# Optimization experiments

Hardware: AMD Instinct MI355X
Metric: run time of the kernel (lower is better)

Reference implementation:

```python
import jax, jax.numpy as jnp
import numpy as np

HIDDEN = 2048
HEADS = 16
HEAD_DIM = HIDDEN // HEADS
GS = 0.1          # governance_strength
ROPE_BASE = 10000.0


def _rope_tables(seq_len, dtype=jnp.float32):
    inv_freq = 1.0 / (ROPE_BASE ** (jnp.arange(0, HEAD_DIM, 2, dtype=jnp.float32) / HEAD_DIM))
    t = jnp.arange(seq_len, dtype=jnp.float32)
    freqs = jnp.outer(t, inv_freq)                      # [S, head_dim/2]
    return jnp.cos(freqs).astype(dtype), jnp.sin(freqs).astype(dtype)


def _apply_rope(x, cos, sin):
    # x: [B, S, H, Dh]; cos/sin: [S, Dh/2] -> broadcast over batch and heads
    c = cos[None, :, None, :]
    s = sin[None, :, None, :]
    x1, x2 = jnp.split(x, 2, axis=-1)
    return jnp.concatenate([x1 * c - x2 * s, x2 * c + x1 * s], axis=-1)


def setup_inputs() -> dict:
    key = jax.random.key(0)
    ks = jax.random.split(key, 9)
    B, S = 2, 1024
    x = jax.random.normal(ks[0], (B, S, HIDDEN), dtype=jnp.float32)
    prophetic_mask = jax.random.normal(ks[1], (B, HEADS, S, S), dtype=jnp.float32)
    policy_mask = jax.random.normal(ks[2], (B, HEADS, S, S), dtype=jnp.float32)
    memory_weights = jax.random.uniform(ks[3], (B, HEADS, S, S), dtype=jnp.float32)
    sd = 1.0 / np.sqrt(HIDDEN)
    Wq = jax.random.normal(ks[4], (HIDDEN, HIDDEN), dtype=jnp.float32) * sd
    Wk = jax.random.normal(ks[5], (HIDDEN, HIDDEN), dtype=jnp.float32) * sd
    Wv = jax.random.normal(ks[6], (HIDDEN, HIDDEN), dtype=jnp.float32) * sd
    Wo = jax.random.normal(ks[7], (HIDDEN, HIDDEN), dtype=jnp.float32) * sd
    bo = jax.random.normal(ks[8], (HIDDEN,), dtype=jnp.float32) * 0.01
    return {"x": x, "prophetic_mask": prophetic_mask, "policy_mask": policy_mask,
            "memory_weights": memory_weights, "Wq": Wq, "Wk": Wk, "Wv": Wv,
            "Wo": Wo, "bo": bo}


def reference(x, prophetic_mask, policy_mask, memory_weights, Wq, Wk, Wv, Wo, bo):
    B, S, D = x.shape
    scale = HEAD_DIM ** -0.5
    # QKV projections (bias=False)
    q = (x @ Wq).reshape(B, S, HEADS, HEAD_DIM)
    k = (x @ Wk).reshape(B, S, HEADS, HEAD_DIM)
    v = (x @ Wv).reshape(B, S, HEADS, HEAD_DIM)
    cos, sin = _rope_tables(S, x.dtype)
    q = _apply_rope(q, cos, sin)
    k = _apply_rope(k, cos, sin)
    # [B, H, S, Dh]
    q = q.transpose(0, 2, 1, 3)
    k = k.transpose(0, 2, 1, 3)
    v = v.transpose(0, 2, 1, 3)
    scores = jnp.einsum('bhqd,bhkd->bhqk', q, k) * scale
    # Combined governance bias: prophetic*gs*0.5 + policy*gs + log(1 + mem*gs + 1e-8)
    bias = (prophetic_mask * (GS * 0.5)
            + policy_mask * GS
            + jnp.log(1.0 + memory_weights * GS + 1e-8))
    scores = scores + bias
    causal = jnp.tril(jnp.ones((S, S), dtype=bool))  # [S, S]
    scores = jnp.where(causal[None, None], scores, -jnp.inf)
    attn = jax.nn.softmax(scores, axis=-1)
    out = jnp.einsum('bhqk,bhkd->bhqd', attn, v)
    out = out.transpose(0, 2, 1, 3).reshape(B, S, D)
    return out @ Wo + bo
```

## Files before the change

### kernel.cpp

```cpp
#include <hip/hip_runtime.h>

typedef unsigned int u32;
typedef unsigned short u16;
typedef __bf16 bf16x8 __attribute__((ext_vector_type(8)));
typedef float f32x4 __attribute__((ext_vector_type(4)));

#define HIDDEN 2048
#define HEADS 16
#define HDIM 128
#define SEQ 1024
#define BATCH 2
#define ROWS (BATCH*SEQ)
#define SCALE 0.08838834764831845f
#define GSC 0.1f

__device__ __forceinline__ u16 f2bf(float f) {
    u32 x = __builtin_bit_cast(u32, f);
    x += 0x7fffu + ((x >> 16) & 1u);
    return (u16)(x >> 16);
}
__device__ __forceinline__ float bf2f(u16 u) {
    return __builtin_bit_cast(float, ((u32)u) << 16);
}
__device__ __forceinline__ void gld_lds16(const void* g, void* l) {
    __builtin_amdgcn_global_load_lds((const __attribute__((address_space(1))) u32*)g,
                                     (__attribute__((address_space(3))) u32*)l, 16, 0, 0);
}

__global__ __launch_bounds__(256) void k_prep(
    const float* __restrict__ x, u16* __restrict__ xb,
    const float* __restrict__ W0, const float* __restrict__ W1,
    const float* __restrict__ W2, const float* __restrict__ W3,
    u16* __restrict__ T0, u16* __restrict__ T1, u16* __restrict__ T2, u16* __restrict__ T3,
    float* __restrict__ cosT, float* __restrict__ sinT) {
    __shared__ float t[32][33];
    const int bid = blockIdx.x;
    const int tid = threadIdx.x;
    if (bid < 4096) {
        const int i = (bid * 256 + tid) * 4;
        float4 v = *(const float4*)(x + i);
        uint2 r;
        r.x = (u32)f2bf(v.x) | ((u32)f2bf(v.y) << 16);
        r.y = (u32)f2bf(v.z) | ((u32)f2bf(v.w) << 16);
        *(uint2*)(xb + i) = r;
    } else if (bid < 4096 + 16384) {
        const int idx = bid - 4096;
        const int bx = (idx & 63) * 32, by = ((idx >> 6) & 63) * 32, z = idx >> 12;
        const float* W = (z == 0) ? W0 : (z == 1) ? W1 : (z == 2) ? W2 : W3;
        u16* Wt = (z == 0) ? T0 : (z == 1) ? T1 : (z == 2) ? T2 : T3;
        const int tx = tid & 31, ty = tid >> 5;
#pragma unroll
        for (int yy = 0; yy < 32; yy += 8)
            t[ty + yy][tx] = W[(size_t)(by + ty + yy) * HIDDEN + bx + tx];
        __syncthreads();
#pragma unroll
        for (int yy = 0; yy < 32; yy += 8)
            Wt[(size_t)(bx + ty + yy) * HIDDEN + by + tx] = f2bf(t[tx][ty + yy]);
    } else {
        const int i = (bid - 20480) * 256 + tid;
        const int s = i >> 6, d = i & 63;
        const float inv = expf(-(float)d * 0.14391156831f);
        const float fr = (float)s * inv;
        cosT[i] = cosf(fr);
        sinT[i] = sinf(fr);
    }
}

__global__ __launch_bounds__(512, 2) void k_qkv(
    const u16* __restrict__ Ag, const u16* __restrict__ Bg,
    u16* __restrict__ qo, u16* __restrict__ ko, u16* __restrict__ vo) {
    __shared__ __align__(16) u16 As[2][16384];
    __shared__ __align__(16) u16 Bs[2][16384];
    const int tid = threadIdx.x;
    const int l = tid & 63, wid = tid >> 6;
    const int wr = wid >> 2, wc = wid & 3;
    const int g = l >> 4, l15 = l & 15;
    const int bid = blockIdx.x;
    const int idx = bid >> 3;
    const int nt = (bid & 7) * 3 + idx % 3;
    const int mt = idx / 3;
    const int m0 = mt * 256, n0 = nt * 256;
    const int swxe = (l15 & 7) << 3;
    int srow[4], scol[4];
#pragma unroll
    for (int p = 0; p < 4; ++p) {
        const int o = p * 8192 + tid * 16;
        const int r = o >> 7;
        srow[p] = r;
        scol[p] = ((o & 127) ^ ((r & 7) << 4)) >> 1;
    }
    f32x4 acc[8][4] = {};
    constexpr int NT = HIDDEN / 64;

#pragma unroll
    for (int p = 0; p < 4; ++p)
        gld_lds16(Ag + (size_t)(m0 + srow[p]) * HIDDEN + scol[p], &As[0][p * 4096 + tid * 8]);
#pragma unroll
    for (int p = 0; p < 4; ++p)
        gld_lds16(Bg + (size_t)(n0 + srow[p]) * HIDDEN + scol[p], &Bs[0][p * 4096 + tid * 8]);
    __syncthreads();

    for (int i = 0; i < NT; ++i) {
        const int cur = i & 1, nb = cur ^ 1;
        if (i + 1 < NT) {
            const int kk1 = (i + 1) * 64;
#pragma unroll
            for (int p = 0; p < 4; ++p)
                gld_lds16(Ag + (size_t)(m0 + srow[p]) * HIDDEN + kk1 + scol[p],
                          &As[nb][p * 4096 + tid * 8]);
#pragma unroll
            for (int p = 0; p < 4; ++p)
                gld_lds16(Bg + (size_t)(n0 + srow[p]) * HIDDEN + kk1 + scol[p],
                          &Bs[nb][p * 4096 + tid * 8]);
        }
        bf16x8 bfr[4][2];
#pragma unroll
        for (int n = 0; n < 4; ++n)
#pragma unroll
            for (int ks = 0; ks < 2; ++ks)
                bfr[n][ks] = *(const bf16x8*)&Bs[cur][(wc * 64 + n * 16 + l15) * 64 +
                                                      ((ks * 32 + g * 8) ^ swxe)];
#pragma unroll
        for (int m = 0; m < 8; ++m) {
            bf16x8 a0 = *(const bf16x8*)&As[cur][(wr * 128 + m * 16 + l15) * 64 +
                                                 ((g * 8) ^ swxe)];
            bf16x8 a1 = *(const bf16x8*)&As[cur][(wr * 128 + m * 16 + l15) * 64 +
                                                 ((32 + g * 8) ^ swxe)];
#pragma unroll
            for (int n = 0; n < 4; ++n) {
                acc[m][n] = __builtin_amdgcn_mfma_f32_16x16x32_bf16(a0, bfr[n][0], acc[m][n], 0, 0, 0);
                acc[m][n] = __builtin_amdgcn_mfma_f32_16x16x32_bf16(a1, bfr[n][1], acc[m][n], 0, 0, 0);
            }
        }
        __syncthreads();
    }
    u16* Cb = (nt < 8) ? qo : (nt < 16) ? ko : vo;
    const int nloc = n0 & 2047;
#pragma unroll
    for (int m = 0; m < 8; ++m)
#pragma unroll
        for (int n = 0; n < 4; ++n) {
            const int col = nloc + wc * 64 + n * 16 + l15;
#pragma unroll
            for (int j = 0; j < 4; ++j) {
                const int row = m0 + wr * 128 + m * 16 + g * 4 + j;
                Cb[(size_t)row * HIDDEN + col] = f2bf(acc[m][n][j]);
            }
        }
}

__global__ __launch_bounds__(256) void k_mid(
    u16* __restrict__ q, u16* __restrict__ k,
    const float* __restrict__ cosT, const float* __restrict__ sinT,
    const u16* __restrict__ v, u16* __restrict__ vT) {
    __shared__ u16 t[32][33];
    const int bid = blockIdx.x;
    const int tid = threadIdx.x;
    if (bid < 8192) {
        const int i = bid * 256 + tid;
        const int row = i >> 10;
        const int hd = i & 1023;
        const int h = hd >> 6, d = hd & 63;
        const int s = row & (SEQ - 1);
        const float c = cosT[s * 64 + d], sn = sinT[s * 64 + d];
        const size_t o1 = (size_t)row * HIDDEN + h * HDIM + d;
        const size_t o2 = o1 + 64;
        float x1 = bf2f(q[o1]), x2 = bf2f(q[o2]);
        q[o1] = f2bf(x1 * c - x2 * sn);
        q[o2] = f2bf(x2 * c + x1 * sn);
        float y1 = bf2f(k[o1]), y2 = bf2f(k[o2]);
        k[o1] = f2bf(y1 * c - y2 * sn);
        k[o2] = f2bf(y2 * c + y1 * sn);
    } else {
        const int idx = bid - 8192;
        const int s0 = (idx & 31) * 32, d0 = ((idx >> 5) & 3) * 32, bh = idx >> 7;
        const int b = bh >> 4, h = bh & 15;
        const int tx = tid & 31, ty = tid >> 5;
#pragma unroll
        for (int yy = 0; yy < 32; yy += 8)
            t[ty + yy][tx] = v[(size_t)(b * SEQ + s0 + ty + yy) * HIDDEN + h * HDIM + d0 + tx];
        __syncthreads();
#pragma unroll
        for (int yy = 0; yy < 32; yy += 8)
            vT[((size_t)bh * HDIM + d0 + ty + yy) * SEQ + s0 + tx] = t[tx][ty + yy];
    }
}

__global__ __launch_bounds__(256) void k_bias(
    const float* __restrict__ pm, const float* __restrict__ po, const float* __restrict__ mw,
    u16* __restrict__ bias) {
    const int j = blockIdx.x;
    const int y = j & 31;
    const int qs = j >> 5;
    const int qt = (qs < 8) ? qs : 23 - qs;
    const int nch = (qt + 1) * 16;
    const int tid = threadIdx.x;
    if (tid >= nch) return;
    const size_t base = ((size_t)y * SEQ + qt * 64) * SEQ + tid * 4;
#pragma unroll 1
    for (int r = 0; r < 64; r += 4) {
        float4 a[4], bq[4], c[4];
#pragma unroll
        for (int rr = 0; rr < 4; ++rr) {
            const size_t off = base + (size_t)(r + rr) * SEQ;
            a[rr]  = *(const float4*)(pm + off);
            bq[rr] = *(const float4*)(po + off);
            c[rr]  = *(const float4*)(mw + off);
        }
#pragma unroll
        for (int rr = 0; rr < 4; ++rr) {
            const size_t off = base + (size_t)(r + rr) * SEQ;
            float v0 = a[rr].x * (GSC * 0.5f) + bq[rr].x * GSC + __logf(fmaf(c[rr].x, GSC, 1.0f + 1e-8f));
            float v1 = a[rr].y * (GSC * 0.5f) + bq[rr].y * GSC + __logf(fmaf(c[rr].y, GSC, 1.0f + 1e-8f));
            float v2 = a[rr].z * (GSC * 0.5f) + bq[rr].z * GSC + __logf(fmaf(c[rr].z, GSC, 1.0f + 1e-8f));
            float v3 = a[rr].w * (GSC * 0.5f) + bq[rr].w * GSC + __logf(fmaf(c[rr].w, GSC, 1.0f + 1e-8f));
            uint2 pk;
            pk.x = (u32)f2bf(v0) | ((u32)f2bf(v1) << 16);
            pk.y = (u32)f2bf(v2) | ((u32)f2bf(v3) << 16);
            *(uint2*)(bias + off) = pk;
        }
    }
}

__global__ __launch_bounds__(128) void k_attn(
    const u16* __restrict__ qraw, const u16* __restrict__ kraw, const u16* __restrict__ vT,
    const u16* __restrict__ bias, u16* __restrict__ attnb) {
    __shared__ __align__(16) u16 Ks[64 * 128];
    __shared__ __align__(16) u16 Vs[128 * 64];
    __shared__ __align__(16) u16 Pl[2][16 * 72];
    const int tid = threadIdx.x;
    const int ln = tid & 63, w = tid >> 6;
    const int g = ln >> 4, q15 = ln & 15;
    const int j = blockIdx.x;
    const int p = j >> 3;
    const int y = (j & 7) * 4 + (p & 3);
    const int t = p >> 2;
    const int hi = t >> 3, lo = t & 7;
    const int qb = hi * 8 + ((hi & 1) ? 7 - lo : lo);
    const int b = y >> 4, h = y & 15;
    const int q0 = qb * 32;
    const int qw = q0 + w * 16;
    const int qg = qw + q15;
    const int ktmax = qb >> 1;
    const int k_r = tid >> 4;
    const int k_c = ((tid & 15) * 8) ^ ((k_r & 7) << 3);
    const int v_r = tid >> 3;
    const int v_c = ((tid & 7) * 8) ^ ((v_r & 7) << 3);
    const int sw = (q15 & 7) << 3;
    bf16x8 qf[4];
    {
        const size_t qoff = (size_t)(b * SEQ + qg) * HIDDEN + h * HDIM;
#pragma unroll
        for (int ds = 0; ds < 4; ++ds) qf[ds] = *(const bf16x8*)(qraw + qoff + ds * 32 + g * 8);
    }
    f32x4 acc_o[8] = {};
    float m_run = -1e30f, l_run = 0.f;
    u16* pw = &Pl[w][0];
    const u16* krow = kraw + (size_t)(b * SEQ) * HIDDEN + h * HDIM;
    const u16* vrow = vT + (size_t)y * HDIM * SEQ;
    const u16* brow = bias + ((size_t)y * SEQ + qg) * SEQ + g * 4;

    uint2 bA[4], bB[4];
    auto issue_bias = [&](uint2 (&bb)[4], int kt) {
        const u16* p0 = brow + kt * 64;
#pragma unroll
        for (int m = 0; m < 4; ++m) bb[m] = *(const uint2*)(p0 + m * 16);
    };

    auto step = [&](int kt, uint2 (&cur)[4], uint2 (&nxt)[4]) {
        const int k0 = kt * 64;
#pragma unroll
        for (int c = 0; c < 8; ++c)
            gld_lds16(krow + (size_t)(k0 + c * 8 + k_r) * HIDDEN + k_c, &Ks[c * 1024 + tid * 8]);
#pragma unroll
        for (int c = 0; c < 8; ++c)
            gld_lds16(vrow + (size_t)(c * 16 + v_r) * SEQ + k0 + v_c, &Vs[c * 1024 + tid * 8]);
        __syncthreads();
        f32x4 accs[4] = {};
#pragma unroll
        for (int ds = 0; ds < 4; ++ds)
#pragma unroll
            for (int m = 0; m < 4; ++m) {
                bf16x8 kf = *(const bf16x8*)&Ks[(m * 16 + q15) * 128 + ((ds * 32 + g * 8) ^ sw)];
                accs[m] = __builtin_amdgcn_mfma_f32_16x16x32_bf16(kf, qf[ds], accs[m], 0, 0, 0);
            }
        if (kt < ktmax) issue_bias(nxt, kt + 1);
        float pmax = -1e30f;
#pragma unroll
        for (int m = 0; m < 4; ++m) {
            const u32 w0 = cur[m].x, w1 = cur[m].y;
            const float bv[4] = { bf2f((u16)(w0 & 0xffff)), bf2f((u16)(w0 >> 16)),
                                  bf2f((u16)(w1 & 0xffff)), bf2f((u16)(w1 >> 16)) };
#pragma unroll
            for (int r = 0; r < 4; ++r) {
                const int kglob = k0 + m * 16 + g * 4 + r;
                float s = (kglob <= qg) ? fmaf(accs[m][r], SCALE, bv[r]) : -1e30f;
                accs[m][r] = s;
                pmax = fmaxf(pmax, s);
            }
        }
        pmax = fmaxf(pmax, __shfl_xor(pmax, 16));
        pmax = fmaxf(pmax, __shfl_xor(pmax, 32));
        const float mnew = fmaxf(m_run, pmax);
        const float alpha = __expf(m_run - mnew);
        float lsum = 0.f;
#pragma unroll
        for (int m = 0; m < 4; ++m)
#pragma unroll
            for (int r = 0; r < 4; ++r) {
                float e = __expf(accs[m][r] - mnew);
                accs[m][r] = e;
                lsum += e;
            }
        lsum += __shfl_xor(lsum, 16);
        lsum += __shfl_xor(lsum, 32);
        l_run = l_run * alpha + lsum;
        m_run = mnew;
#pragma unroll
        for (int m = 0; m < 4; ++m) {
            uint2 pk;
            pk.x = (u32)f2bf(accs[m][0]) | ((u32)f2bf(accs[m][1]) << 16);
            pk.y = (u32)f2bf(accs[m][2]) | ((u32)f2bf(accs[m][3]) << 16);
            *(uint2*)&pw[q15 * 72 + m * 16 + g * 4] = pk;
        }
        float al[4];
#pragma unroll
        for (int jj = 0; jj < 4; ++jj) al[jj] = __shfl(alpha, g * 4 + jj);
#pragma unroll
        for (int n = 0; n < 8; ++n)
#pragma unroll
            for (int jj = 0; jj < 4; ++jj) acc_o[n][jj] *= al[jj];
#pragma unroll
        for (int c = 0; c < 2; ++c) {
            const bf16x8 af = *(const bf16x8*)&pw[q15 * 72 + c * 32 + g * 8];
#pragma unroll
            for (int n = 0; n < 8; ++n) {
                const bf16x8 vf = *(const bf16x8*)&Vs[(n * 16 + q15) * 64 + ((c * 32 + g * 8) ^ sw)];
                acc_o[n] = __builtin_amdgcn_mfma_f32_16x16x32_bf16(af, vf, acc_o[n], 0, 0, 0);
            }
        }
        __syncthreads();
    };

    issue_bias(bA, 0);
    int kt = 0;
    for (;;) {
        step(kt, bA, bB);
        if (kt == ktmax) break;
        ++kt;
        step(kt, bB, bA);
        if (kt == ktmax) break;
        ++kt;
    }

    const float linv = 1.0f / l_run;
    float li[4];
#pragma unroll
    for (int jj = 0; jj < 4; ++jj) li[jj] = __shfl(linv, g * 4 + jj);
#pragma unroll
    for (int n = 0; n < 8; ++n)
#pragma unroll
        for (int jj = 0; jj < 4; ++jj) {
            const int row = b * SEQ + qw + g * 4 + jj;
            const int col = h * HDIM + n * 16 + q15;
            attnb[(size_t)row * HIDDEN + col] = f2bf(acc_o[n][jj] * li[jj]);
        }
}

__global__ __launch_bounds__(256) void k_out(
    const u16* __restrict__ A, const u16* __restrict__ Bt,
    float* __restrict__ Cf, const float* __restrict__ bias) {
    constexpr int K = HIDDEN, N = HIDDEN;
    __shared__ __align__(16) u16 As[128 * 64];
    __shared__ __align__(16) u16 Bs[128 * 64];
    const int tid = threadIdx.x;
    const int ln = tid & 63, w = tid >> 6;
    const int wr = w >> 1, wc = w & 1;
    const int g = ln >> 4, l15 = ln & 15;
    const int m0 = blockIdx.x * 128, n0 = blockIdx.y * 128;
    const int srow = tid >> 3, scol = (tid & 7) * 8;
    f32x4 acc[4][4] = {};
    for (int kk = 0; kk < K; kk += 64) {
#pragma unroll
        for (int c = 0; c < 4; ++c) {
            gld_lds16(A + (size_t)(m0 + c * 32 + srow) * K + kk + scol, &As[c * 2048 + tid * 8]);
            gld_lds16(Bt + (size_t)(n0 + c * 32 + srow) * K + kk + scol, &Bs[c * 2048 + tid * 8]);
        }
        __syncthreads();
#pragma unroll
        for (int ks = 0; ks < 2; ++ks) {
            bf16x8 a[4], b[4];
#pragma unroll
            for (int m = 0; m < 4; ++m)
                a[m] = *(const bf16x8*)&As[(wr * 64 + m * 16 + l15) * 64 + ks * 32 + g * 8];
#pragma unroll
            for (int n = 0; n < 4; ++n)
                b[n] = *(const bf16x8*)&Bs[(wc * 64 + n * 16 + l15) * 64 + ks * 32 + g * 8];
#pragma unroll
            for (int m = 0; m < 4; ++m)
#pragma unroll
                for (int n = 0; n < 4; ++n)
                    acc[m][n] = __builtin_amdgcn_mfma_f32_16x16x32_bf16(a[m], b[n], acc[m][n], 0, 0, 0);
        }
        __syncthreads();
    }
#pragma unroll
    for (int m = 0; m < 4; ++m)
#pragma unroll
        for (int n = 0; n < 4; ++n) {
            const int col = n0 + wc * 64 + n * 16 + l15;
#pragma unroll
            for (int j = 0; j < 4; ++j) {
                const int row = m0 + wr * 64 + m * 16 + g * 4 + j;
                Cf[(size_t)row * N + col] = acc[m][n][j] + bias[col];
            }
        }
}

extern "C" void kernel_launch(void* const* d_in, const int* in_sizes, int n_in,
                              void* d_out, int out_size, void* d_ws, size_t ws_size,
                              hipStream_t stream) {
    (void)in_sizes; (void)n_in; (void)out_size; (void)ws_size;
    const float* x  = (const float*)d_in[0];
    const float* pm = (const float*)d_in[1];
    const float* po = (const float*)d_in[2];
    const float* mw = (const float*)d_in[3];
    const float* Wq = (const float*)d_in[4];
    const float* Wk = (const float*)d_in[5];
    const float* Wv = (const float*)d_in[6];
    const float* Wo = (const float*)d_in[7];
    const float* bo = (const float*)d_in[8];
    float* out = (float*)d_out;

    char* ws = (char*)d_ws;
    const size_t SZ = (size_t)ROWS * HIDDEN;
    const size_t OFF = SZ * 2;
    u16* xb    = (u16*)(ws + 0 * OFF);
    u16* Wqt   = (u16*)(ws + 1 * OFF);
    u16* Wkt   = (u16*)(ws + 2 * OFF);
    u16* Wvt   = (u16*)(ws + 3 * OFF);
    u16* Wot   = (u16*)(ws + 4 * OFF);
    u16* qrawp = (u16*)(ws + 5 * OFF);
    u16* krawp = (u16*)(ws + 6 * OFF);
    u16* vrawp = (u16*)(ws + 7 * OFF);
    u16* vTp   = (u16*)(ws + 8 * OFF);
    u16* attnb = (u16*)(ws + 9 * OFF);
    float* cosT = (float*)(ws + 10 * OFF);
    float* sinT = (float*)(ws + 10 * OFF + 262144);
    u16* biasb  = (u16*)(ws + 11 * OFF);

    k_prep<<<dim3(20736), 256, 0, stream>>>(x, xb, Wq, Wk, Wv, Wo,
                                            Wqt, Wkt, Wvt, Wot, cosT, sinT);
    k_qkv<<<dim3(192), 512, 0, stream>>>(xb, Wqt, qrawp, krawp, vrawp);
    k_mid<<<dim3(12288), 256, 0, stream>>>(qrawp, krawp, cosT, sinT, vrawp, vTp);
    k_bias<<<dim3(512), 256, 0, stream>>>(pm, po, mw, biasb);
    k_attn<<<dim3(1024), 128, 0, stream>>>(qrawp, krawp, vTp, biasb, attnb);
    k_out<<<dim3(16, 16), 256, 0, stream>>>(attnb, Wot, out, bo);
}
```

Measured before the change: 259.0 us.

## Rebalance bias kernel grid and double-buffer swizzled LDS in output GEMM

The bias kernel now gives each block 16 query rows, with rows-per-thread work proportional to the causal width, launched over 2048 blocks instead of 512. This replaces the old 64-row tiles in which many threads sat idle. The output projection GEMM gains double-buffered LDS with prefetch of the next k-tile, an XOR swizzle against LDS bank conflicts, and a remapped 1D grid for better tile locality. The changes target memory-bound bias generation and load/compute serialization in the GEMM, at the cost of twice the LDS use in k_out.

```diff
diff --git a/kernel.cpp b/kernel.cpp
--- a/kernel.cpp
+++ b/kernel.cpp
@@ -190,35 +190,29 @@
     const float* __restrict__ pm, const float* __restrict__ po, const float* __restrict__ mw,
     u16* __restrict__ bias) {
     const int j = blockIdx.x;
+    const int t = 63 - (j >> 5);
     const int y = j & 31;
-    const int qs = j >> 5;
-    const int qt = (qs < 8) ? qs : 23 - qs;
-    const int nch = (qt + 1) * 16;
-    const int tid = threadIdx.x;
-    if (tid >= nch) return;
-    const size_t base = ((size_t)y * SEQ + qt * 64) * SEQ + tid * 4;
-#pragma unroll 1
-    for (int r = 0; r < 64; r += 4) {
-        float4 a[4], bq[4], c[4];
-#pragma unroll
-        for (int rr = 0; rr < 4; ++rr) {
-            const size_t off = base + (size_t)(r + rr) * SEQ;
-            a[rr]  = *(const float4*)(pm + off);
-            bq[rr] = *(const float4*)(po + off);
-            c[rr]  = *(const float4*)(mw + off);
-        }
-#pragma unroll
-        for (int rr = 0; rr < 4; ++rr) {
-            const size_t off = base + (size_t)(r + rr) * SEQ;
-            float v0 = a[rr].x * (GSC * 0.5f) + bq[rr].x * GSC + __logf(fmaf(c[rr].x, GSC, 1.0f + 1e-8f));
-            float v1 = a[rr].y * (GSC * 0.5f) + bq[rr].y * GSC + __logf(fmaf(c[rr].y, GSC, 1.0f + 1e-8f));
-            float v2 = a[rr].z * (GSC * 0.5f) + bq[rr].z * GSC + __logf(fmaf(c[rr].z, GSC, 1.0f + 1e-8f));
-            float v3 = a[rr].w * (GSC * 0.5f) + bq[rr].w * GSC + __logf(fmaf(c[rr].w, GSC, 1.0f + 1e-8f));
-            uint2 pk;
-            pk.x = (u32)f2bf(v0) | ((u32)f2bf(v1) << 16);
-            pk.y = (u32)f2bf(v2) | ((u32)f2bf(v3) << 16);
-            *(uint2*)(bias + off) = pk;
-        }
+    const int row = t * 16 + (threadIdx.x >> 4);
+    const int c0 = threadIdx.x & 15;
+    const int C = 4 * t + 4;
+    const size_t rbase = ((size_t)y * SEQ + row) * SEQ;
+    const float* pr = pm + rbase;
+    const float* qr = po + rbase;
+    const float* mr = mw + rbase;
+    u16* br = bias + rbase;
+#pragma unroll 2
+    for (int c = c0; c < C; c += 16) {
+        const float4 a = *(const float4*)(pr + c * 4);
+        const float4 b = *(const float4*)(qr + c * 4);
+        const float4 m = *(const float4*)(mr + c * 4);
+        float v0 = a.x * (GSC * 0.5f) + b.x * GSC + __logf(fmaf(m.x, GSC, 1.0f + 1e-8f));
+        float v1 = a.y * (GSC * 0.5f) + b.y * GSC + __logf(fmaf(m.y, GSC, 1.0f + 1e-8f));
+        float v2 = a.z * (GSC * 0.5f) + b.z * GSC + __logf(fmaf(m.z, GSC, 1.0f + 1e-8f));
+        float v3 = a.w * (GSC * 0.5f) + b.w * GSC + __logf(fmaf(m.w, GSC, 1.0f + 1e-8f));
+        uint2 pk;
+        pk.x = (u32)f2bf(v0) | ((u32)f2bf(v1) << 16);
+        pk.y = (u32)f2bf(v2) | ((u32)f2bf(v3) << 16);
+        *(uint2*)(br + c * 4) = pk;
     }
 }
 
@@ -370,37 +364,65 @@
 __global__ __launch_bounds__(256) void k_out(
     const u16* __restrict__ A, const u16* __restrict__ Bt,
     float* __restrict__ Cf, const float* __restrict__ bias) {
-    constexpr int K = HIDDEN, N = HIDDEN;
-    __shared__ __align__(16) u16 As[128 * 64];
-    __shared__ __align__(16) u16 Bs[128 * 64];
+    __shared__ __align__(16) u16 As[2][8192];
+    __shared__ __align__(16) u16 Bs[2][8192];
     const int tid = threadIdx.x;
-    const int ln = tid & 63, w = tid >> 6;
-    const int wr = w >> 1, wc = w & 1;
-    const int g = ln >> 4, l15 = ln & 15;
-    const int m0 = blockIdx.x * 128, n0 = blockIdx.y * 128;
-    const int srow = tid >> 3, scol = (tid & 7) * 8;
+    const int l = tid & 63, wid = tid >> 6;
+    const int wr = wid >> 1, wc = wid & 1;
+    const int g = l >> 4, l15 = l & 15;
+    const int bid = blockIdx.x;
+    const int rr = (bid & 7) * 32 + (bid >> 3);
+    const int mt = rr >> 4, nt = rr & 15;
+    const int m0 = mt * 128, n0 = nt * 128;
+    const int swxe = (l15 & 7) << 3;
+    int srow[4], scol[4];
+#pragma unroll
+    for (int p = 0; p < 4; ++p) {
+        const int o = p * 4096 + tid * 16;
+        const int r = o >> 7;
+        srow[p] = r;
+        scol[p] = ((o & 127) ^ ((r & 7) << 4)) >> 1;
+    }
     f32x4 acc[4][4] = {};
-    for (int kk = 0; kk < K; kk += 64) {
-#pragma unroll
-        for (int c = 0; c < 4; ++c) {
-            gld_lds16(A + (size_t)(m0 + c * 32 + srow) * K + kk + scol, &As[c * 2048 + tid * 8]);
-            gld_lds16(Bt + (size_t)(n0 + c * 32 + srow) * K + kk + scol, &Bs[c * 2048 + tid * 8]);
-        }
-        __syncthreads();
-#pragma unroll
-        for (int ks = 0; ks < 2; ++ks) {
-            bf16x8 a[4], b[4];
-#pragma unroll
-            for (int m = 0; m < 4; ++m)
-                a[m] = *(const bf16x8*)&As[(wr * 64 + m * 16 + l15) * 64 + ks * 32 + g * 8];
-#pragma unroll
-            for (int n = 0; n < 4; ++n)
-                b[n] = *(const bf16x8*)&Bs[(wc * 64 + n * 16 + l15) * 64 + ks * 32 + g * 8];
-#pragma unroll
-            for (int m = 0; m < 4; ++m)
-#pragma unroll
-                for (int n = 0; n < 4; ++n)
-                    acc[m][n] = __builtin_amdgcn_mfma_f32_16x16x32_bf16(a[m], b[n], acc[m][n], 0, 0, 0);
+    constexpr int NT = HIDDEN / 64;
+
+#pragma unroll
+    for (int p = 0; p < 4; ++p) {
+        gld_lds16(A + (size_t)(m0 + srow[p]) * HIDDEN + scol[p], &As[0][p * 2048 + tid * 8]);
+        gld_lds16(Bt + (size_t)(n0 + srow[p]) * HIDDEN + scol[p], &Bs[0][p * 2048 + tid * 8]);
+    }
+    __syncthreads();
+
+    for (int i = 0; i < NT; ++i) {
+        const int cur = i & 1, nb = cur ^ 1;
+        if (i + 1 < NT) {
+            const int kk1 = (i + 1) * 64;
+#pragma unroll
+            for (int p = 0; p < 4; ++p) {
+                gld_lds16(A + (size_t)(m0 + srow[p]) * HIDDEN + kk1 + scol[p],
+                          &As[nb][p * 2048 + tid * 8]);
+                gld_lds16(Bt + (size_t)(n0 + srow[p]) * HIDDEN + kk1 + scol[p],
+                          &Bs[nb][p * 2048 + tid * 8]);
+            }
+        }
+        bf16x8 bfr[4][2];
+#pragma unroll
+        for (int n = 0; n < 4; ++n)
+#pragma unroll
+            for (int ks = 0; ks < 2; ++ks)
+                bfr[n][ks] = *(const bf16x8*)&Bs[cur][(wc * 64 + n * 16 + l15) * 64 +
+                                                      ((ks * 32 + g * 8) ^ swxe)];
+#pragma unroll
+        for (int m = 0; m < 4; ++m) {
+            bf16x8 a0 = *(const bf16x8*)&As[cur][(wr * 64 + m * 16 + l15) * 64 +
+                                                 ((g * 8) ^ swxe)];
+            bf16x8 a1 = *(const bf16x8*)&As[cur][(wr * 64 + m * 16 + l15) * 64 +
+                                                 ((32 + g * 8) ^ swxe)];
+#pragma unroll
+            for (int n = 0; n < 4; ++n) {
+                acc[m][n] = __builtin_amdgcn_mfma_f32_16x16x32_bf16(a0, bfr[n][0], acc[m][n], 0, 0, 0);
+                acc[m][n] = __builtin_amdgcn_mfma_f32_16x16x32_bf16(a1, bfr[n][1], acc[m][n], 0, 0, 0);
+            }
         }
         __syncthreads();
     }
@@ -412,7 +434,7 @@
 #pragma unroll
             for (int j = 0; j < 4; ++j) {
                 const int row = m0 + wr * 64 + m * 16 + g * 4 + j;
-                Cf[(size_t)row * N + col] = acc[m][n][j] + bias[col];
+                Cf[(size_t)row * HIDDEN + col] = acc[m][n][j] + bias[col];
             }
         }
 }
@@ -453,7 +475,7 @@
                                             Wqt, Wkt, Wvt, Wot, cosT, sinT);
     k_qkv<<<dim3(192), 512, 0, stream>>>(xb, Wqt, qrawp, krawp, vrawp);
     k_mid<<<dim3(12288), 256, 0, stream>>>(qrawp, krawp, cosT, sinT, vrawp, vTp);
-    k_bias<<<dim3(512), 256, 0, stream>>>(pm, po, mw, biasb);
+    k_bias<<<dim3(2048), 256, 0, stream>>>(pm, po, mw, biasb);
     k_attn<<<dim3(1024), 128, 0, stream>>>(qrawp, krawp, vTp, biasb, attnb);
-    k_out<<<dim3(16, 16), 256, 0, stream>>>(attnb, Wot, out, bo);
-}
+    k_out<<<dim3(256), 256, 0, stream>>>(attnb, Wot, out, bo);
+}
```

Measured after the change: 253.0 us. 2.3% less time.
